# Kernel tuning notes

Hardware: AMD Instinct MI355X
Metric: run time of the kernel (lower is better)

The kernel has to match this reference:

```python
import jax, jax.numpy as jnp
import numpy as np

T, B, D_IN, H, N_OUT = 512, 256, 85, 512, 33

def setup_inputs() -> dict:
    key = jax.random.key(0)
    ks = jax.random.split(key, 16)
    s_in = 1.0 / np.sqrt(D_IN)
    s_h = 1.0 / np.sqrt(H)
    def u(k, shape, s):
        return jax.random.uniform(k, shape, jnp.float32, -s, s)
    return {
        "x": jax.random.normal(ks[0], (T, B, D_IN), jnp.float32),
        "Wxi": u(ks[1], (H, D_IN), s_in),
        "Wxf": u(ks[2], (H, D_IN), s_in),
        "Wxo": u(ks[3], (H, D_IN), s_in),
        "Wxc": u(ks[4], (H, D_IN), s_in),
        "Whi": u(ks[5], (H, H), s_h), "bhi": u(ks[6], (H,), s_h),
        "Whf": u(ks[7], (H, H), s_h), "bhf": u(ks[8], (H,), s_h),
        "Who": u(ks[9], (H, H), s_h), "bho": u(ks[10], (H,), s_h),
        "Whc": u(ks[11], (H, H), s_h), "bhc": u(ks[12], (H,), s_h),
        "Wro": u(ks[13], (N_OUT, H), s_h), "bro": u(ks[14], (N_OUT,), s_h),
    }

def _lstm(x, Wxi, Wxf, Wxo, Wxc, Whi, bhi, Whf, bhf, Who, bho, Whc, bhc, Wro, bro):
    act = jnp.tanh  # hp['activation'] == 'tanh'
    # Precompute all input-side projections in one big GEMM-like pass: [T,B,H]
    xi = jnp.einsum('tbi,hi->tbh', x, Wxi)
    xf = jnp.einsum('tbi,hi->tbh', x, Wxf)
    xo = jnp.einsum('tbi,hi->tbh', x, Wxo)
    xc = jnp.einsum('tbi,hi->tbh', x, Wxc)
    Bsz = x.shape[1]
    Hd = Whi.shape[0]
    C0 = jnp.zeros((Bsz, Hd), x.dtype)
    H0 = jnp.zeros((Bsz, Hd), x.dtype)

    def step(carry, xs):
        C, Hs = carry
        xi_t, xf_t, xo_t, xc_t = xs
        I = jax.nn.sigmoid(xi_t + Hs @ Whi.T + bhi)
        F = jax.nn.sigmoid(xf_t + Hs @ Whf.T + bhf)
        O = jax.nn.sigmoid(xo_t + Hs @ Who.T + bho)
        C_hat = act(xc_t + Hs @ Whc.T + bhc)
        C = F * C + I * C_hat
        Hs = O * act(C)
        return (C, Hs), Hs

    _, hidden_states = jax.lax.scan(step, (C0, H0), (xi, xf, xo, xc))
    # readout over all timesteps: [T,B,n_output]
    return jnp.einsum('tbh,oh->tbo', hidden_states, Wro) + bro

def reference(x, Wxi, Wxf, Wxo, Wxc, Whi, bhi, Whf, bhf, Who, bho, Whc, bhc, Wro, bro):
    return _lstm(x, Wxi, Wxf, Wxo, Wxc, Whi, bhi, Whf, bhf, Who, bho, Whc, bhc, Wro, bro)
```

## Files before the change

kernel.cpp:

```cpp
#include <hip/hip_runtime.h>
#include <hip/hip_bf16.h>
#include <stdint.h>

#define T_STEPS 512
#define BATCH   256
#define DIN     85
#define HDIM    512
#define NOUT    33

#define BBLK  16
#define HS    32
#define LDA   1040
#define LDX   208

#define SENT  0x7FC07FC0u

typedef __attribute__((ext_vector_type(8))) short s8v;
typedef __attribute__((ext_vector_type(4))) float f4v;
typedef __attribute__((ext_vector_type(4))) uint32_t u32x4;

__device__ __forceinline__ uint16_t f2bf(float f) {
    uint32_t x = __builtin_bit_cast(uint32_t, f);
    uint32_t r = (x + 0x7fffu + ((x >> 16) & 1u)) >> 16;
    return (uint16_t)r;
}
__device__ __forceinline__ float sigm(float v) {
    v = fminf(fmaxf(v, -30.f), 30.f);
    return 1.f / (1.f + __expf(-v));
}
__device__ __forceinline__ float tanh_f(float v) {
    v = fminf(fmaxf(v, -15.f), 15.f);
    float e = __expf(2.f * v);
    return (e - 1.f) / (e + 1.f);
}
__device__ __forceinline__ s8v cvt8(const float* p) {
    s8v v;
#pragma unroll
    for (int j = 0; j < 8; ++j) v[j] = (short)f2bf(p[j]);
    return v;
}

__device__ __forceinline__ void issue4_dev(u32x4& v, const uint32_t* p) {
    asm volatile("global_load_dwordx4 %0, %1, off sc0 sc1"
                 : "+v"(v) : "v"(p) : "memory");
}
__device__ __forceinline__ void wait_vm1(u32x4& a, u32x4& b, u32x4& c, u32x4& d) {
    asm volatile("s_waitcnt vmcnt(1)"
                 : "+v"(a), "+v"(b), "+v"(c), "+v"(d) :: "memory");
}
__device__ __forceinline__ void wait_vm0(u32x4& a, u32x4& b, u32x4& c, u32x4& d) {
    asm volatile("s_waitcnt vmcnt(0)"
                 : "+v"(a), "+v"(b), "+v"(c), "+v"(d) :: "memory");
}
__device__ __forceinline__ uint32_t has_sent(const u32x4& v) {
    return (uint32_t)(v[0] == SENT) | (uint32_t)(v[1] == SENT) |
           (uint32_t)(v[2] == SENT) | (uint32_t)(v[3] == SENT);
}

__global__ __launch_bounds__(256) void lstm_init(uint32_t* __restrict__ hbuf)
{
    const size_t n4 = (size_t)(T_STEPS + 1) * BATCH * HDIM / 2 / 4;
    u32x4 s; s[0] = SENT; s[1] = SENT; s[2] = SENT; s[3] = SENT;
    u32x4* p = (u32x4*)hbuf;
    for (size_t i = (size_t)blockIdx.x * 256 + threadIdx.x; i < n4;
         i += (size_t)gridDim.x * 256)
        p[i] = s;
}

__global__ __launch_bounds__(256, 1) void lstm_rec(
    const float* __restrict__ x,
    const float* __restrict__ Wxi, const float* __restrict__ Wxf,
    const float* __restrict__ Wxo, const float* __restrict__ Wxc,
    const float* __restrict__ Whi, const float* __restrict__ bhi,
    const float* __restrict__ Whf, const float* __restrict__ bhf,
    const float* __restrict__ Who, const float* __restrict__ bho,
    const float* __restrict__ Whc, const float* __restrict__ bhc,
    uint16_t* __restrict__ hbuf)
{
    __shared__ __align__(16) uint8_t hA[16 * LDA];
    __shared__ __align__(16) uint8_t xA[16 * LDX];
    __shared__ float gbuf[4 * 16 * 33];

    const int tid  = threadIdx.x;
    const int bid  = blockIdx.x;
    const int xcd  = bid & 7;
    const int slot = bid >> 3;
    const int grp  = xcd * 2 + (slot >> 4);
    const int mem  = slot & 15;
    const int b0   = grp * BBLK;
    const int hs   = mem * HS;

    const int wave  = tid >> 6;
    const int lane  = tid & 63;
    const int col16 = lane & 15;
    const int quad  = lane >> 4;

    const float* Wh  = (wave == 0) ? Whi : (wave == 1) ? Whf : (wave == 2) ? Who : Whc;
    const float* Wxp = (wave == 0) ? Wxi : (wave == 1) ? Wxf : (wave == 2) ? Wxo : Wxc;

    s8v bh[2][16];
#pragma unroll
    for (int nt = 0; nt < 2; ++nt) {
        const float* rowp = Wh + (size_t)(hs + nt * 16 + col16) * HDIM;
#pragma unroll
        for (int kt = 0; kt < 16; ++kt)
            bh[nt][kt] = cvt8(rowp + kt * 32 + quad * 8);
    }
    s8v bx[2][3];
#pragma unroll
    for (int nt = 0; nt < 2; ++nt) {
        const float* rowp = Wxp + (size_t)(hs + nt * 16 + col16) * DIN;
#pragma unroll
        for (int kt = 0; kt < 3; ++kt) {
            s8v v;
#pragma unroll
            for (int j = 0; j < 8; ++j) {
                int k = kt * 32 + quad * 8 + j;
                v[j] = (k < DIN) ? (short)f2bf(rowp[k]) : (short)0;
            }
            bx[nt][kt] = v;
        }
    }

    const int r  = tid >> 4;
    const int c0 = (tid & 15) * 2;
    const float bi0 = bhi[hs + c0], bi1 = bhi[hs + c0 + 1];
    const float bf0 = bhf[hs + c0], bf1 = bhf[hs + c0 + 1];
    const float bo0 = bho[hs + c0], bo1 = bho[hs + c0 + 1];
    const float bc0 = bhc[hs + c0], bc1 = bhc[hs + c0 + 1];
    float C0 = 0.f, C1 = 0.f;

    uint32_t* hbuf32 = (uint32_t*)hbuf;
    const size_t hslot = ((size_t)(b0 + r) * HDIM + hs + c0) >> 1;

    const int rrow[4] = { tid >> 6, (tid + 256) >> 6, (tid + 512) >> 6, (tid + 768) >> 6 };
    const int rc8     = tid & 63;
    const uint32_t ownm = (rc8 >= mem * 4 && rc8 < mem * 4 + 4) ? 1u : 0u;

    float xreg[6];
    auto load_x = [&](int t) {
#pragma unroll
        for (int j = 0; j < 6; ++j) {
            int v = tid + j * 256;
            int row = v / 96, k = v % 96;
            xreg[j] = (k < DIN) ? x[(size_t)(t * BATCH + b0 + row) * DIN + k] : 0.f;
        }
    };
    auto store_x = [&]() {
#pragma unroll
        for (int j = 0; j < 6; ++j) {
            int v = tid + j * 256;
            int row = v / 96, k = v % 96;
            *(uint16_t*)(xA + row * LDX + k * 2) = f2bf(xreg[j]);
        }
    };

    load_x(0);
    for (int j = tid; j < 16 * LDA / 16; j += 256) {
        s8v z;
#pragma unroll
        for (int q = 0; q < 8; ++q) z[q] = 0;
        ((s8v*)hA)[j] = z;
    }
    store_x();
    __syncthreads();

    u32x4 v0 = {SENT, SENT, SENT, SENT};
    u32x4 v1 = v0, v2 = v0, v3 = v0;

    for (int t = 0; t < T_STEPS; ++t) {
        const int last = (t == T_STEPS - 1);

        if (!last) load_x(t + 1);

        f4v acc0 = {0.f, 0.f, 0.f, 0.f}, acc1 = {0.f, 0.f, 0.f, 0.f};
#pragma unroll
        for (int kt = 0; kt < 16; ++kt) {
            s8v a = *(const s8v*)(hA + col16 * LDA + kt * 64 + quad * 16);
            acc0 = __builtin_amdgcn_mfma_f32_16x16x32_bf16(a, bh[0][kt], acc0, 0, 0, 0);
            acc1 = __builtin_amdgcn_mfma_f32_16x16x32_bf16(a, bh[1][kt], acc1, 0, 0, 0);
        }
#pragma unroll
        for (int kt = 0; kt < 3; ++kt) {
            s8v a = *(const s8v*)(xA + col16 * LDX + kt * 64 + quad * 16);
            acc0 = __builtin_amdgcn_mfma_f32_16x16x32_bf16(a, bx[0][kt], acc0, 0, 0, 0);
            acc1 = __builtin_amdgcn_mfma_f32_16x16x32_bf16(a, bx[1][kt], acc1, 0, 0, 0);
        }
#pragma unroll
        for (int rr = 0; rr < 4; ++rr) {
            int b = quad * 4 + rr;
            gbuf[(wave * 16 + b) * 33 + col16]      = acc0[rr];
            gbuf[(wave * 16 + b) * 33 + 16 + col16] = acc1[rr];
        }

        __syncthreads();

        const uint32_t* src = hbuf32 + (size_t)(t + 1) * (BATCH * HDIM / 2)
                                     + (size_t)b0 * (HDIM / 2);
        const uint32_t* p0 = src + (size_t)rrow[0] * (HDIM / 2) + rc8 * 4;
        const uint32_t* p1 = src + (size_t)rrow[1] * (HDIM / 2) + rc8 * 4;
        const uint32_t* p2 = src + (size_t)rrow[2] * (HDIM / 2) + rc8 * 4;
        const uint32_t* p3 = src + (size_t)rrow[3] * (HDIM / 2) + rc8 * 4;

        if (!last && !ownm) {
            issue4_dev(v0, p0); issue4_dev(v1, p1);
            issue4_dev(v2, p2); issue4_dev(v3, p3);
        }

        float pi0 = gbuf[(0 * 16 + r) * 33 + c0] + bi0;
        float pi1 = gbuf[(0 * 16 + r) * 33 + c0 + 1] + bi1;
        float pf0 = gbuf[(1 * 16 + r) * 33 + c0] + bf0;
        float pf1 = gbuf[(1 * 16 + r) * 33 + c0 + 1] + bf1;
        float po0 = gbuf[(2 * 16 + r) * 33 + c0] + bo0;
        float po1 = gbuf[(2 * 16 + r) * 33 + c0 + 1] + bo1;
        float pc0 = gbuf[(3 * 16 + r) * 33 + c0] + bc0;
        float pc1 = gbuf[(3 * 16 + r) * 33 + c0 + 1] + bc1;

        float I0 = sigm(pi0), F0 = sigm(pf0), O0 = sigm(po0), G0 = tanh_f(pc0);
        float I1 = sigm(pi1), F1 = sigm(pf1), O1 = sigm(po1), G1 = tanh_f(pc1);
        C0 = F0 * C0 + I0 * G0;
        C1 = F1 * C1 + I1 * G1;
        float h0 = O0 * tanh_f(C0);
        float h1 = O1 * tanh_f(C1);

        uint32_t packed = (uint32_t)f2bf(h0) | ((uint32_t)f2bf(h1) << 16);
        __hip_atomic_store(&hbuf32[(size_t)(t + 1) * (BATCH * HDIM / 2) + hslot],
                           packed, __ATOMIC_RELAXED, __HIP_MEMORY_SCOPE_AGENT);

        if (last) break;

        *(uint32_t*)(hA + r * LDA + (hs + c0) * 2) = packed;

        store_x();

        wait_vm1(v0, v1, v2, v3);
        uint32_t s0 = ownm ? 0u : has_sent(v0);
        uint32_t s1 = ownm ? 0u : has_sent(v1);
        uint32_t s2 = ownm ? 0u : has_sent(v2);
        uint32_t s3 = ownm ? 0u : has_sent(v3);
        int round = 0;
        while (s0 | s1 | s2 | s3) {
            if (++round > 50000) break;
            if (round >= 6) __builtin_amdgcn_s_sleep(2);
            if (s0) issue4_dev(v0, p0);
            if (s1) issue4_dev(v1, p1);
            if (s2) issue4_dev(v2, p2);
            if (s3) issue4_dev(v3, p3);
            wait_vm0(v0, v1, v2, v3);
            s0 = has_sent(v0); s1 = has_sent(v1);
            s2 = has_sent(v2); s3 = has_sent(v3);
        }
        if (!ownm) {
            *(u32x4*)(hA + rrow[0] * LDA + rc8 * 16) = v0;
            *(u32x4*)(hA + rrow[1] * LDA + rc8 * 16) = v1;
            *(u32x4*)(hA + rrow[2] * LDA + rc8 * 16) = v2;
            *(u32x4*)(hA + rrow[3] * LDA + rc8 * 16) = v3;
        }

        __syncthreads();
    }
}

__global__ __launch_bounds__(256, 1) void lstm_out(
    const uint16_t* __restrict__ hbuf,
    const float* __restrict__ Wro, const float* __restrict__ bro,
    float* __restrict__ out)
{
    __shared__ __align__(16) uint8_t hT[64 * LDA];

    const int tid   = threadIdx.x;
    const int bid   = blockIdx.x;
    const int wave  = tid >> 6;
    const int lane  = tid & 63;
    const int col16 = lane & 15;
    const int quad  = lane >> 4;

    s8v bw[3][16];
    float bias[3];
#pragma unroll
    for (int nt = 0; nt < 3; ++nt) {
        int o = nt * 16 + col16;
        bias[nt] = (o < NOUT) ? bro[o] : 0.f;
#pragma unroll
        for (int kt = 0; kt < 16; ++kt) {
            if (o < NOUT) {
                bw[nt][kt] = cvt8(Wro + (size_t)o * HDIM + kt * 32 + quad * 8);
            } else {
                s8v z;
#pragma unroll
                for (int q = 0; q < 8; ++q) z[q] = 0;
                bw[nt][kt] = z;
            }
        }
    }

    const uint16_t* hsrc = hbuf + (size_t)BATCH * HDIM;

    for (int sub = 0; sub < 8; ++sub) {
        size_t row0 = (size_t)bid * 512 + (size_t)sub * 64;
#pragma unroll
        for (int j = 0; j < 16; ++j) {
            int v = tid + j * 256;
            int row = v >> 6, c8 = v & 63;
            s8v val = *(const s8v*)(hsrc + (row0 + row) * HDIM + c8 * 8);
            *(s8v*)(hT + row * LDA + c8 * 16) = val;
        }
        __syncthreads();

        f4v acc[3];
#pragma unroll
        for (int nt = 0; nt < 3; ++nt) acc[nt] = (f4v){0.f, 0.f, 0.f, 0.f};
#pragma unroll
        for (int kt = 0; kt < 16; ++kt) {
            s8v a = *(const s8v*)(hT + (wave * 16 + col16) * LDA + kt * 64 + quad * 16);
#pragma unroll
            for (int nt = 0; nt < 3; ++nt)
                acc[nt] = __builtin_amdgcn_mfma_f32_16x16x32_bf16(a, bw[nt][kt], acc[nt], 0, 0, 0);
        }
#pragma unroll
        for (int nt = 0; nt < 3; ++nt) {
            int o = nt * 16 + col16;
            if (o < NOUT) {
#pragma unroll
                for (int rr = 0; rr < 4; ++rr) {
                    size_t rg = row0 + (size_t)wave * 16 + quad * 4 + rr;
                    out[rg * NOUT + o] = acc[nt][rr] + bias[nt];
                }
            }
        }
        __syncthreads();
    }
}

extern "C" void kernel_launch(void* const* d_in, const int* in_sizes, int n_in,
                              void* d_out, int out_size, void* d_ws, size_t ws_size,
                              hipStream_t stream)
{
    const float* x   = (const float*)d_in[0];
    const float* Wxi = (const float*)d_in[1];
    const float* Wxf = (const float*)d_in[2];
    const float* Wxo = (const float*)d_in[3];
    const float* Wxc = (const float*)d_in[4];
    const float* Whi = (const float*)d_in[5];
    const float* bhi = (const float*)d_in[6];
    const float* Whf = (const float*)d_in[7];
    const float* bhf = (const float*)d_in[8];
    const float* Who = (const float*)d_in[9];
    const float* bho = (const float*)d_in[10];
    const float* Whc = (const float*)d_in[11];
    const float* bhc = (const float*)d_in[12];
    const float* Wro = (const float*)d_in[13];
    const float* bro = (const float*)d_in[14];
    float* out = (float*)d_out;

    uint16_t* hbuf = (uint16_t*)d_ws;

    lstm_init<<<2048, 256, 0, stream>>>((uint32_t*)hbuf);
    lstm_rec<<<256, 256, 0, stream>>>(x, Wxi, Wxf, Wxo, Wxc,
                                      Whi, bhi, Whf, bhf, Who, bho, Whc, bhc,
                                      hbuf);
    lstm_out<<<256, 256, 0, stream>>>(hbuf, Wro, bro, out);
}
```

Before: 1.250 ms.

## Merge two hidden-slice blocks into one 512-thread block for recurrent LSTM

Each recurrent block now owns 64 hidden units (two 32-column members) for a 16-row batch group, running 8 waves instead of 4. The grid halves to 128 blocks. Each thread now polls two 16-byte chunks instead of four, and the sentinel-based cross-block exchange covers 8 peer blocks instead of 16. This cuts the number of global spin-wait loads per step and the inter-block synchronisation fan-in. In exchange it uses fewer CUs, and each block does twice the MFMA and activation work per step.

Measured after the change: 1.680 ms. +34.4%, slower.

```diff
diff --git a/kernel.cpp b/kernel.cpp
--- a/kernel.cpp
+++ b/kernel.cpp
@@ -44,13 +44,13 @@
     asm volatile("global_load_dwordx4 %0, %1, off sc0 sc1"
                  : "+v"(v) : "v"(p) : "memory");
 }
-__device__ __forceinline__ void wait_vm1(u32x4& a, u32x4& b, u32x4& c, u32x4& d) {
+__device__ __forceinline__ void wait_vm1(u32x4& a, u32x4& b) {
     asm volatile("s_waitcnt vmcnt(1)"
-                 : "+v"(a), "+v"(b), "+v"(c), "+v"(d) :: "memory");
-}
-__device__ __forceinline__ void wait_vm0(u32x4& a, u32x4& b, u32x4& c, u32x4& d) {
+                 : "+v"(a), "+v"(b) :: "memory");
+}
+__device__ __forceinline__ void wait_vm0(u32x4& a, u32x4& b) {
     asm volatile("s_waitcnt vmcnt(0)"
-                 : "+v"(a), "+v"(b), "+v"(c), "+v"(d) :: "memory");
+                 : "+v"(a), "+v"(b) :: "memory");
 }
 __device__ __forceinline__ uint32_t has_sent(const u32x4& v) {
     return (uint32_t)(v[0] == SENT) | (uint32_t)(v[1] == SENT) |
@@ -67,7 +67,7 @@
         p[i] = s;
 }
 
-__global__ __launch_bounds__(256, 1) void lstm_rec(
+__global__ __launch_bounds__(512, 1) void lstm_rec(
     const float* __restrict__ x,
     const float* __restrict__ Wxi, const float* __restrict__ Wxf,
     const float* __restrict__ Wxo, const float* __restrict__ Wxc,
@@ -79,24 +79,27 @@
 {
     __shared__ __align__(16) uint8_t hA[16 * LDA];
     __shared__ __align__(16) uint8_t xA[16 * LDX];
-    __shared__ float gbuf[4 * 16 * 33];
+    __shared__ float gbuf[2][4 * 16 * 33];
 
     const int tid  = threadIdx.x;
     const int bid  = blockIdx.x;
     const int xcd  = bid & 7;
     const int slot = bid >> 3;
-    const int grp  = xcd * 2 + (slot >> 4);
-    const int mem  = slot & 15;
+    const int grp  = xcd * 2 + (slot >> 3);
+    const int blkm = slot & 7;
     const int b0   = grp * BBLK;
-    const int hs   = mem * HS;
+    const int bslice = blkm * 64;
 
     const int wave  = tid >> 6;
+    const int memb  = wave >> 2;
+    const int gate  = wave & 3;
     const int lane  = tid & 63;
     const int col16 = lane & 15;
     const int quad  = lane >> 4;
-
-    const float* Wh  = (wave == 0) ? Whi : (wave == 1) ? Whf : (wave == 2) ? Who : Whc;
-    const float* Wxp = (wave == 0) ? Wxi : (wave == 1) ? Wxf : (wave == 2) ? Wxo : Wxc;
+    const int hs    = bslice + memb * HS;
+
+    const float* Wh  = (gate == 0) ? Whi : (gate == 1) ? Whf : (gate == 2) ? Who : Whc;
+    const float* Wxp = (gate == 0) ? Wxi : (gate == 1) ? Wxf : (gate == 2) ? Wxo : Wxc;
 
     s8v bh[2][16];
 #pragma unroll
@@ -122,41 +125,45 @@
         }
     }
 
-    const int r  = tid >> 4;
-    const int c0 = (tid & 15) * 2;
-    const float bi0 = bhi[hs + c0], bi1 = bhi[hs + c0 + 1];
-    const float bf0 = bhf[hs + c0], bf1 = bhf[hs + c0 + 1];
-    const float bo0 = bho[hs + c0], bo1 = bho[hs + c0 + 1];
-    const float bc0 = bhc[hs + c0], bc1 = bhc[hs + c0 + 1];
+    const int pm   = tid >> 8;
+    const int t256 = tid & 255;
+    const int r    = t256 >> 4;
+    const int c0l  = (t256 & 15) * 2;
+    const int gcol = bslice + pm * HS + c0l;
+    const float bi0 = bhi[gcol], bi1 = bhi[gcol + 1];
+    const float bf0 = bhf[gcol], bf1 = bhf[gcol + 1];
+    const float bo0 = bho[gcol], bo1 = bho[gcol + 1];
+    const float bc0 = bhc[gcol], bc1 = bhc[gcol + 1];
     float C0 = 0.f, C1 = 0.f;
 
     uint32_t* hbuf32 = (uint32_t*)hbuf;
-    const size_t hslot = ((size_t)(b0 + r) * HDIM + hs + c0) >> 1;
-
-    const int rrow[4] = { tid >> 6, (tid + 256) >> 6, (tid + 512) >> 6, (tid + 768) >> 6 };
-    const int rc8     = tid & 63;
-    const uint32_t ownm = (rc8 >= mem * 4 && rc8 < mem * 4 + 4) ? 1u : 0u;
-
-    float xreg[6];
+    const size_t hslot = ((size_t)(b0 + r) * HDIM + gcol) >> 1;
+
+    const int prow0 = tid >> 6;
+    const int prow1 = prow0 + 8;
+    const int rc8   = tid & 63;
+    const uint32_t ownm = ((uint32_t)(rc8 >> 3) == (uint32_t)blkm) ? 1u : 0u;
+
+    float xreg[3];
     auto load_x = [&](int t) {
 #pragma unroll
-        for (int j = 0; j < 6; ++j) {
-            int v = tid + j * 256;
+        for (int j = 0; j < 3; ++j) {
+            int v = tid + j * 512;
             int row = v / 96, k = v % 96;
             xreg[j] = (k < DIN) ? x[(size_t)(t * BATCH + b0 + row) * DIN + k] : 0.f;
         }
     };
     auto store_x = [&]() {
 #pragma unroll
-        for (int j = 0; j < 6; ++j) {
-            int v = tid + j * 256;
+        for (int j = 0; j < 3; ++j) {
+            int v = tid + j * 512;
             int row = v / 96, k = v % 96;
             *(uint16_t*)(xA + row * LDX + k * 2) = f2bf(xreg[j]);
         }
     };
 
     load_x(0);
-    for (int j = tid; j < 16 * LDA / 16; j += 256) {
+    for (int j = tid; j < 16 * LDA / 16; j += 512) {
         s8v z;
 #pragma unroll
         for (int q = 0; q < 8; ++q) z[q] = 0;
@@ -166,7 +173,7 @@
     __syncthreads();
 
     u32x4 v0 = {SENT, SENT, SENT, SENT};
-    u32x4 v1 = v0, v2 = v0, v3 = v0;
+    u32x4 v1 = v0;
 
     for (int t = 0; t < T_STEPS; ++t) {
         const int last = (t == T_STEPS - 1);
@@ -189,32 +196,29 @@
 #pragma unroll
         for (int rr = 0; rr < 4; ++rr) {
             int b = quad * 4 + rr;
-            gbuf[(wave * 16 + b) * 33 + col16]      = acc0[rr];
-            gbuf[(wave * 16 + b) * 33 + 16 + col16] = acc1[rr];
+            gbuf[memb][(gate * 16 + b) * 33 + col16]      = acc0[rr];
+            gbuf[memb][(gate * 16 + b) * 33 + 16 + col16] = acc1[rr];
         }
 
         __syncthreads();
 
         const uint32_t* src = hbuf32 + (size_t)(t + 1) * (BATCH * HDIM / 2)
                                      + (size_t)b0 * (HDIM / 2);
-        const uint32_t* p0 = src + (size_t)rrow[0] * (HDIM / 2) + rc8 * 4;
-        const uint32_t* p1 = src + (size_t)rrow[1] * (HDIM / 2) + rc8 * 4;
-        const uint32_t* p2 = src + (size_t)rrow[2] * (HDIM / 2) + rc8 * 4;
-        const uint32_t* p3 = src + (size_t)rrow[3] * (HDIM / 2) + rc8 * 4;
+        const uint32_t* p0 = src + (size_t)prow0 * (HDIM / 2) + rc8 * 4;
+        const uint32_t* p1 = src + (size_t)prow1 * (HDIM / 2) + rc8 * 4;
 
         if (!last && !ownm) {
             issue4_dev(v0, p0); issue4_dev(v1, p1);
-            issue4_dev(v2, p2); issue4_dev(v3, p3);
-        }
-
-        float pi0 = gbuf[(0 * 16 + r) * 33 + c0] + bi0;
-        float pi1 = gbuf[(0 * 16 + r) * 33 + c0 + 1] + bi1;
-        float pf0 = gbuf[(1 * 16 + r) * 33 + c0] + bf0;
-        float pf1 = gbuf[(1 * 16 + r) * 33 + c0 + 1] + bf1;
-        float po0 = gbuf[(2 * 16 + r) * 33 + c0] + bo0;
-        float po1 = gbuf[(2 * 16 + r) * 33 + c0 + 1] + bo1;
-        float pc0 = gbuf[(3 * 16 + r) * 33 + c0] + bc0;
-        float pc1 = gbuf[(3 * 16 + r) * 33 + c0 + 1] + bc1;
+        }
+
+        float pi0 = gbuf[pm][(0 * 16 + r) * 33 + c0l] + bi0;
+        float pi1 = gbuf[pm][(0 * 16 + r) * 33 + c0l + 1] + bi1;
+        float pf0 = gbuf[pm][(1 * 16 + r) * 33 + c0l] + bf0;
+        float pf1 = gbuf[pm][(1 * 16 + r) * 33 + c0l + 1] + bf1;
+        float po0 = gbuf[pm][(2 * 16 + r) * 33 + c0l] + bo0;
+        float po1 = gbuf[pm][(2 * 16 + r) * 33 + c0l + 1] + bo1;
+        float pc0 = gbuf[pm][(3 * 16 + r) * 33 + c0l] + bc0;
+        float pc1 = gbuf[pm][(3 * 16 + r) * 33 + c0l + 1] + bc1;
 
         float I0 = sigm(pi0), F0 = sigm(pf0), O0 = sigm(po0), G0 = tanh_f(pc0);
         float I1 = sigm(pi1), F1 = sigm(pf1), O1 = sigm(po1), G1 = tanh_f(pc1);
@@ -229,32 +233,25 @@
 
         if (last) break;
 
-        *(uint32_t*)(hA + r * LDA + (hs + c0) * 2) = packed;
+        *(uint32_t*)(hA + r * LDA + gcol * 2) = packed;
 
         store_x();
 
-        wait_vm1(v0, v1, v2, v3);
+        wait_vm1(v0, v1);
         uint32_t s0 = ownm ? 0u : has_sent(v0);
         uint32_t s1 = ownm ? 0u : has_sent(v1);
-        uint32_t s2 = ownm ? 0u : has_sent(v2);
-        uint32_t s3 = ownm ? 0u : has_sent(v3);
         int round = 0;
-        while (s0 | s1 | s2 | s3) {
+        while (s0 | s1) {
             if (++round > 50000) break;
             if (round >= 6) __builtin_amdgcn_s_sleep(2);
             if (s0) issue4_dev(v0, p0);
             if (s1) issue4_dev(v1, p1);
-            if (s2) issue4_dev(v2, p2);
-            if (s3) issue4_dev(v3, p3);
-            wait_vm0(v0, v1, v2, v3);
+            wait_vm0(v0, v1);
             s0 = has_sent(v0); s1 = has_sent(v1);
-            s2 = has_sent(v2); s3 = has_sent(v3);
         }
         if (!ownm) {
-            *(u32x4*)(hA + rrow[0] * LDA + rc8 * 16) = v0;
-            *(u32x4*)(hA + rrow[1] * LDA + rc8 * 16) = v1;
-            *(u32x4*)(hA + rrow[2] * LDA + rc8 * 16) = v2;
-            *(u32x4*)(hA + rrow[3] * LDA + rc8 * 16) = v3;
+            *(u32x4*)(hA + prow0 * LDA + rc8 * 16) = v0;
+            *(u32x4*)(hA + prow1 * LDA + rc8 * 16) = v1;
         }
 
         __syncthreads();
@@ -356,7 +353,7 @@
     uint16_t* hbuf = (uint16_t*)d_ws;
 
     lstm_init<<<2048, 256, 0, stream>>>((uint32_t*)hbuf);
-    lstm_rec<<<256, 256, 0, stream>>>(x, Wxi, Wxf, Wxo, Wxc,
+    lstm_rec<<<128, 512, 0, stream>>>(x, Wxi, Wxf, Wxo, Wxc,
                                       Whi, bhi, Whf, bhf, Who, bho, Whc, bhc,
                                       hbuf);
     lstm_out<<<256, 256, 0, stream>>>(hbuf, Wro, bro, out);
```
